# Optimization experiments

Measured on AMD Instinct MI355X. Metric: run time of the kernel, lower is better.

## Reference

```python
import jax, jax.numpy as jnp
import numpy as np


def setup_inputs() -> dict:
    key = jax.random.key(0)
    k1, k2, k3, k4, k5 = jax.random.split(key, 5)
    B, S, H, NL = 256, 128, 768, 2
    return {
        "t_logits": jax.random.normal(k1, (B, NL), dtype=jnp.float32),
        "s_logits": jax.random.normal(k2, (B, NL), dtype=jnp.float32),
        "t_features": jax.random.normal(k3, (B, S, H), dtype=jnp.float32),
        "s_features": jax.random.normal(k4, (B, S, H), dtype=jnp.float32),
        "labels": jax.random.randint(k5, (B,), 0, NL, dtype=jnp.int64),
        "k": 5,
        "temperature": 4,
    }


def reference(t_logits, s_logits, t_features, s_features, labels, k, temperature):
    B = s_features.shape[0]
    D = s_features.shape[1] * s_features.shape[2]  # flattened feature dim S*H
    T = jnp.asarray(temperature, dtype=s_logits.dtype)

    # train_loss: standard cross-entropy computed inside the student model
    logp = jax.nn.log_softmax(s_logits, axis=-1)
    train_loss = -jnp.mean(jnp.take_along_axis(logp, labels[:, None].astype(jnp.int32), axis=1))

    # soft_loss: KL(batchmean) between temperature-softened teacher/student
    soft_targets = jax.nn.softmax(t_logits / T, axis=-1)
    log_probs = jax.nn.log_softmax(s_logits / T, axis=-1)
    soft_loss = jnp.sum(soft_targets * (jnp.log(soft_targets) - log_probs)) / B * T * T

    # distill_loss: per-sample squared distances to label-matched teacher
    # features, take k nearest (self included, dist 0), sum of per-neighbor
    # MSE = sqdist / D.
    tf = t_features.reshape(B, -1)
    sf = s_features.reshape(B, -1)
    # ||s_i - t_j||^2 via GEMM: [B, B]
    sq = (jnp.sum(sf * sf, axis=1)[:, None]
          + jnp.sum(tf * tf, axis=1)[None, :]
          - 2.0 * sf @ tf.T)
    sq = jnp.maximum(sq, 0.0)
    same = labels[:, None] == labels[None, :]
    masked = jnp.where(same, sq, jnp.inf)
    neg_top, _ = jax.lax.top_k(-masked, k)  # k smallest distances per row
    vals = -neg_top
    valid = jnp.isfinite(vals)  # handles groups smaller than k
    distill_loss = jnp.sum(jnp.where(valid, vals, 0.0)) / D

    return train_loss, soft_loss, distill_loss
```

## Files before the change

kernel.cpp:

```cpp
#include <hip/hip_runtime.h>
#include <math.h>


#define BM 128
#define BN 128
#define BKF 32
#define NS 8

typedef __attribute__((ext_vector_type(8))) short short8;
typedef __attribute__((ext_vector_type(4))) float f32x4;

__device__ inline void async16(const float* g, float* l) {
    __builtin_amdgcn_global_load_lds(
        (const __attribute__((address_space(1))) void*)g,
        (__attribute__((address_space(3))) void*)l,
        16, 0, 0);
}

__device__ inline unsigned pack_trunc(float a, float b) {
    return (__float_as_uint(a) >> 16) | (__float_as_uint(b) & 0xffff0000u);
}

union U8 { short8 v; unsigned u[4]; };

__global__ __launch_bounds__(256) void gemm_dot_kernel(const float* __restrict__ S,
                                                       const float* __restrict__ T,
                                                       float* __restrict__ part,
                                                       float* __restrict__ spart,
                                                       float* __restrict__ tpart,
                                                       int B, int K, int KC) {
    __shared__ __align__(16) float As[BM * BKF];
    __shared__ __align__(16) float Bs[BN * BKF];

    const int tid  = threadIdx.x;
    const int i0   = blockIdx.x * BM;
    const int j0   = blockIdx.y * BN;
    const int bz   = blockIdx.z;
    const int kbeg = bz * KC;
    const int kend = kbeg + KC;

    const int lane = tid & 63;
    const int wid  = tid >> 6;
    const int wm   = wid >> 1;
    const int wn   = wid & 1;
    const int l15  = lane & 15;
    const int quad = lane >> 4;

    const int rl = lane >> 3;
    const int p  = lane & 7;
    const float* srcA[4];
    const float* srcB[4];
    float* dstA[4];
    float* dstB[4];
    #pragma unroll
    for (int j = 0; j < 4; ++j) {
        const int c   = wid * 4 + j;
        const int row = c * 8 + rl;
        const int g   = p ^ (row & 7);
        int gi = i0 + row; if (gi >= B) gi = B - 1;
        int gj = j0 + row; if (gj >= B) gj = B - 1;
        srcA[j] = S + (size_t)gi * K + kbeg + g * 4;
        srcB[j] = T + (size_t)gj * K + kbeg + g * 4;
        dstA[j] = &As[c * 256];
        dstB[j] = &Bs[c * 256];
    }

    int aoff[4], boff[4];
    #pragma unroll
    for (int t = 0; t < 4; ++t) {
        const int ra = wm * 64 + t * 16 + l15;
        aoff[t] = ra * BKF + (((2 * quad) ^ (ra & 7)) * 4);
        const int rb = wn * 64 + t * 16 + l15;
        boff[t] = rb * BKF + (((2 * quad) ^ (rb & 7)) * 4);
    }

    const bool doS = (blockIdx.y == 0);
    const bool doT = (blockIdx.x == 0);
    const int  rn  = tid >> 1;
    const int  hn  = tid & 1;

    f32x4 acc[4][4] = {};
    float pns = 0.f, pnt = 0.f;

    for (int kb = kbeg; kb < kend; kb += BKF) {
        __syncthreads();
        #pragma unroll
        for (int j = 0; j < 4; ++j) {
            async16(srcA[j], dstA[j]);
            async16(srcB[j], dstB[j]);
            srcA[j] += BKF;
            srcB[j] += BKF;
        }
        __syncthreads();

        if (doS) {
            #pragma unroll
            for (int j = 0; j < 4; ++j) {
                const int pos = hn * 4 + ((j + rn) & 3);
                f32x4 v = *(const f32x4*)&As[rn * BKF + pos * 4];
                pns += v.x * v.x + v.y * v.y + v.z * v.z + v.w * v.w;
            }
        }
        if (doT) {
            #pragma unroll
            for (int j = 0; j < 4; ++j) {
                const int pos = hn * 4 + ((j + rn) & 3);
                f32x4 v = *(const f32x4*)&Bs[rn * BKF + pos * 4];
                pnt += v.x * v.x + v.y * v.y + v.z * v.z + v.w * v.w;
            }
        }

        short8 af[4], bf[4];
        #pragma unroll
        for (int t = 0; t < 4; ++t) {
            f32x4 va = *(const f32x4*)&As[aoff[t]];
            f32x4 vb = *(const f32x4*)&As[aoff[t] ^ 4];
            U8 u;
            u.u[0] = pack_trunc(va.x, va.y);
            u.u[1] = pack_trunc(va.z, va.w);
            u.u[2] = pack_trunc(vb.x, vb.y);
            u.u[3] = pack_trunc(vb.z, vb.w);
            af[t] = u.v;
        }
        #pragma unroll
        for (int t = 0; t < 4; ++t) {
            f32x4 va = *(const f32x4*)&Bs[boff[t]];
            f32x4 vb = *(const f32x4*)&Bs[boff[t] ^ 4];
            U8 u;
            u.u[0] = pack_trunc(va.x, va.y);
            u.u[1] = pack_trunc(va.z, va.w);
            u.u[2] = pack_trunc(vb.x, vb.y);
            u.u[3] = pack_trunc(vb.z, vb.w);
            bf[t] = u.v;
        }
        #pragma unroll
        for (int mi = 0; mi < 4; ++mi)
            #pragma unroll
            for (int ni = 0; ni < 4; ++ni)
                acc[mi][ni] = __builtin_amdgcn_mfma_f32_16x16x32_bf16(
                    af[mi], bf[ni], acc[mi][ni], 0, 0, 0);
    }

    float* outp = part + (size_t)bz * B * B;
    #pragma unroll
    for (int mi = 0; mi < 4; ++mi) {
        #pragma unroll
        for (int ni = 0; ni < 4; ++ni) {
            #pragma unroll
            for (int r = 0; r < 4; ++r) {
                const int ig = i0 + wm * 64 + mi * 16 + quad * 4 + r;
                const int jg = j0 + wn * 64 + ni * 16 + l15;
                if (ig < B && jg < B)
                    outp[(size_t)ig * B + jg] = acc[mi][ni][r];
            }
        }
    }

    if (doS) {
        float v = pns + __shfl_xor(pns, 1, 64);
        if (hn == 0 && i0 + rn < B) spart[(size_t)bz * B + i0 + rn] = v;
    }
    if (doT) {
        float v = pnt + __shfl_xor(pnt, 1, 64);
        if (hn == 0 && j0 + rn < B) tpart[(size_t)bz * B + j0 + rn] = v;
    }
}

__global__ __launch_bounds__(256) void reduce_kernel(const float* __restrict__ part,
                                                     const float* __restrict__ spart,
                                                     const float* __restrict__ tpart,
                                                     float* __restrict__ part2,
                                                     float* __restrict__ snorm2,
                                                     float* __restrict__ tnorm2,
                                                     int n, int B, int gz) {
    const int s  = blockIdx.y;
    const int bx = blockIdx.x;
    const int t  = threadIdx.x;
    if ((int)bx * 256 < n) {
        const int idx = bx * 256 + t;
        if (idx < n) {
            float a = 0.f;
            for (int z = s; z < gz; z += NS)
                a += part[(size_t)z * n + idx];
            part2[(size_t)s * n + idx] = a;
        }
    } else {
        if (t < B) {
            float a = 0.f, b = 0.f;
            for (int z = s; z < gz; z += NS) {
                a += spart[(size_t)z * B + t];
                b += tpart[(size_t)z * B + t];
            }
            snorm2[s * B + t] = a;
            tnorm2[s * B + t] = b;
        }
    }
}

__global__ __launch_bounds__(256) void tail_kernel(const float* __restrict__ part2,
                                                   const float* __restrict__ snorm2,
                                                   const float* __restrict__ tnorm2,
                                                   const float* __restrict__ t_logits,
                                                   const float* __restrict__ s_logits,
                                                   const int* __restrict__ labels,
                                                   const int* __restrict__ kp,
                                                   const int* __restrict__ tp,
                                                   float* __restrict__ rowsum,
                                                   int* __restrict__ counter,
                                                   float* __restrict__ out,
                                                   int B, int K, int NL) {
    const int i   = blockIdx.x;
    const int tid = threadIdx.x;
    const size_t BB = (size_t)B * B;

    __shared__ float svals[256];
    __shared__ float rv[256];
    __shared__ int   ri[256];
    __shared__ int   lastf;

    float v = INFINITY;
    if (tid < B && labels[i] == labels[tid]) {
        float dt = 0.f, sn = 0.f, tn = 0.f;
        #pragma unroll
        for (int s = 0; s < NS; ++s) {
            dt += part2[(size_t)s * BB + (size_t)i * B + tid];
            sn += snorm2[s * B + i];
            tn += tnorm2[s * B + tid];
        }
        v = fmaxf(sn + tn - 2.0f * dt, 0.0f);
    }
    svals[tid] = v;
    __syncthreads();

    const int k = kp[0];
    float sum = 0.0f;
    for (int it = 0; it < k; ++it) {
        rv[tid] = svals[tid];
        ri[tid] = tid;
        __syncthreads();
        #pragma unroll
        for (int s = 128; s > 0; s >>= 1) {
            if (tid < s) {
                if (rv[tid + s] < rv[tid]) { rv[tid] = rv[tid + s]; ri[tid] = ri[tid + s]; }
            }
            __syncthreads();
        }
        if (tid == 0) {
            if (rv[0] < 3.0e38f) sum += rv[0];
            svals[ri[0]] = INFINITY;
        }
        __syncthreads();
    }

    if (tid == 0) {
        rowsum[i] = sum;
        __threadfence();
        lastf = (atomicAdd(counter, 1) == B - 1) ? 1 : 0;
    }
    __syncthreads();
    if (!lastf) return;

    __threadfence();
    const float Tv = (float)tp[0];
    float rs = (tid < B) ? rowsum[tid] : 0.f;
    float ce = 0.0f, kl = 0.0f;
    for (int s = tid; s < B; s += 256) {
        const float* sl = s_logits + (size_t)s * NL;
        const float* tl = t_logits + (size_t)s * NL;
        float mx = -INFINITY;
        for (int c = 0; c < NL; ++c) mx = fmaxf(mx, sl[c]);
        float se = 0.0f;
        for (int c = 0; c < NL; ++c) se += expf(sl[c] - mx);
        ce += logf(se) + mx - sl[labels[s]];

        float mxs = -INFINITY, mxt = -INFINITY;
        for (int c = 0; c < NL; ++c) {
            mxs = fmaxf(mxs, sl[c] / Tv);
            mxt = fmaxf(mxt, tl[c] / Tv);
        }
        float ses = 0.0f, set = 0.0f;
        for (int c = 0; c < NL; ++c) {
            ses += expf(sl[c] / Tv - mxs);
            set += expf(tl[c] / Tv - mxt);
        }
        float lses = logf(ses) + mxs;
        float lset = logf(set) + mxt;
        for (int c = 0; c < NL; ++c) {
            float lst = tl[c] / Tv - lset;
            float ls  = sl[c] / Tv - lses;
            kl += expf(lst) * (lst - ls);
        }
    }
    #pragma unroll
    for (int off = 32; off > 0; off >>= 1) {
        ce += __shfl_down(ce, off, 64);
        kl += __shfl_down(kl, off, 64);
        rs += __shfl_down(rs, off, 64);
    }
    __shared__ float wce[4], wkl[4], wrs[4];
    if ((tid & 63) == 0) { wce[tid >> 6] = ce; wkl[tid >> 6] = kl; wrs[tid >> 6] = rs; }
    __syncthreads();
    if (tid == 0) {
        out[0] = (wce[0] + wce[1] + wce[2] + wce[3]) / (float)B;
        out[1] = (wkl[0] + wkl[1] + wkl[2] + wkl[3]) / (float)B * Tv * Tv;
        out[2] = (wrs[0] + wrs[1] + wrs[2] + wrs[3]) / (float)K;
    }
}

extern "C" void kernel_launch(void* const* d_in, const int* in_sizes, int n_in,
                              void* d_out, int out_size, void* d_ws, size_t ws_size,
                              hipStream_t stream) {
    const float* t_logits = (const float*)d_in[0];
    const float* s_logits = (const float*)d_in[1];
    const float* t_feat   = (const float*)d_in[2];
    const float* s_feat   = (const float*)d_in[3];
    const int*   labels   = (const int*)d_in[4];
    const int*   kp       = (const int*)d_in[5];
    const int*   tp       = (const int*)d_in[6];
    float* out = (float*)d_out;

    const int B  = in_sizes[4];
    const int NL = in_sizes[0] / B;
    const int K  = in_sizes[2] / B;
    const size_t BB = (size_t)B * B;

    const size_t avail = ws_size / 4;
    const int cands[] = {192, 256, 128, 96, 64, 48, 32, 24, 16, 12, 8, 6, 4, 3, 2, 1};
    int gz = 1;
    for (int ci = 0; ci < 16; ++ci) {
        const int g = cands[ci];
        if (K % (g * BKF) != 0) continue;
        const size_t need = (size_t)g * BB + (size_t)NS * BB
                          + 2 * (size_t)g * B + 2 * (size_t)NS * B + B + 1;
        if (need <= avail) { gz = g; break; }
    }
    const int KC = K / gz;

    float* ws      = (float*)d_ws;
    float* part    = ws;
    float* part2   = part + (size_t)gz * BB;
    float* spart   = part2 + (size_t)NS * BB;
    float* tpart   = spart + (size_t)gz * B;
    float* snorm2  = tpart + (size_t)gz * B;
    float* tnorm2  = snorm2 + (size_t)NS * B;
    float* rowsum  = tnorm2 + (size_t)NS * B;
    int*   counter = (int*)(rowsum + B);

    hipMemsetAsync(counter, 0, sizeof(int), stream);

    dim3 grid((B + BM - 1) / BM, (B + BN - 1) / BN, gz);
    gemm_dot_kernel<<<grid, 256, 0, stream>>>(s_feat, t_feat, part, spart, tpart,
                                              B, K, KC);

    dim3 grid2((unsigned)(BB / 256 + 1), NS);
    reduce_kernel<<<grid2, 256, 0, stream>>>(part, spart, tpart, part2,
                                             snorm2, tnorm2, (int)BB, B, gz);

    tail_kernel<<<B, 256, 0, stream>>>(part2, snorm2, tnorm2, t_logits, s_logits,
                                       labels, kp, tp, rowsum, counter, out,
                                       B, K, NL);
}
```

Measured before the change: 277.1 us.

## Double-buffer GEMM LDS loads, drop reduce kernel, fold split-K sum into tail

The GEMM now double-buffers its LDS tiles: it prefetches the next K-slice with async global-to-LDS loads while the MFMAs run on the current one, which removes one barrier per iteration. The separate reduce kernel and the memset are removed. The counter is zeroed inside the GEMM, and the tail kernel sums all gz split-K partials directly. This saves two launches and a full intermediate write and read, but each tail thread now performs gz strided loads. It also assumes the counter reset is visible before the tail runs, which stream ordering provides.

```diff
diff --git a/kernel.cpp b/kernel.cpp
--- a/kernel.cpp
+++ b/kernel.cpp
@@ -5,7 +5,7 @@
 #define BM 128
 #define BN 128
 #define BKF 32
-#define NS 8
+#define STAGE (BM * BKF)
 
 typedef __attribute__((ext_vector_type(8))) short short8;
 typedef __attribute__((ext_vector_type(4))) float f32x4;
@@ -28,9 +28,9 @@
                                                        float* __restrict__ part,
                                                        float* __restrict__ spart,
                                                        float* __restrict__ tpart,
+                                                       int* __restrict__ counter,
                                                        int B, int K, int KC) {
-    __shared__ __align__(16) float As[BM * BKF];
-    __shared__ __align__(16) float Bs[BN * BKF];
+    extern __shared__ __align__(16) float smem[];
 
     const int tid  = threadIdx.x;
     const int i0   = blockIdx.x * BM;
@@ -39,6 +39,9 @@
     const int kbeg = bz * KC;
     const int kend = kbeg + KC;
 
+    if (blockIdx.x == 0 && blockIdx.y == 0 && bz == 0 && tid == 0)
+        *counter = 0;
+
     const int lane = tid & 63;
     const int wid  = tid >> 6;
     const int wm   = wid >> 1;
@@ -50,8 +53,7 @@
     const int p  = lane & 7;
     const float* srcA[4];
     const float* srcB[4];
-    float* dstA[4];
-    float* dstB[4];
+    int dstOff[4];
     #pragma unroll
     for (int j = 0; j < 4; ++j) {
         const int c   = wid * 4 + j;
@@ -61,8 +63,7 @@
         int gj = j0 + row; if (gj >= B) gj = B - 1;
         srcA[j] = S + (size_t)gi * K + kbeg + g * 4;
         srcB[j] = T + (size_t)gj * K + kbeg + g * 4;
-        dstA[j] = &As[c * 256];
-        dstB[j] = &Bs[c * 256];
+        dstOff[j] = c * 256;
     }
 
     int aoff[4], boff[4];
@@ -82,16 +83,36 @@
     f32x4 acc[4][4] = {};
     float pns = 0.f, pnt = 0.f;
 
+    {
+        float* As0 = smem;
+        float* Bs0 = smem + STAGE;
+        #pragma unroll
+        for (int j = 0; j < 4; ++j) {
+            async16(srcA[j], &As0[dstOff[j]]);
+            async16(srcB[j], &Bs0[dstOff[j]]);
+            srcA[j] += BKF;
+            srcB[j] += BKF;
+        }
+    }
+
+    int par = 0;
     for (int kb = kbeg; kb < kend; kb += BKF) {
         __syncthreads();
-        #pragma unroll
-        for (int j = 0; j < 4; ++j) {
-            async16(srcA[j], dstA[j]);
-            async16(srcB[j], dstB[j]);
-            srcA[j] += BKF;
-            srcB[j] += BKF;
-        }
-        __syncthreads();
+
+        if (kb + BKF < kend) {
+            float* Asn = smem + (par ^ 1) * 2 * STAGE;
+            float* Bsn = Asn + STAGE;
+            #pragma unroll
+            for (int j = 0; j < 4; ++j) {
+                async16(srcA[j], &Asn[dstOff[j]]);
+                async16(srcB[j], &Bsn[dstOff[j]]);
+                srcA[j] += BKF;
+                srcB[j] += BKF;
+            }
+        }
+
+        const float* As = smem + par * 2 * STAGE;
+        const float* Bs = As + STAGE;
 
         if (doS) {
             #pragma unroll
@@ -139,6 +160,8 @@
             for (int ni = 0; ni < 4; ++ni)
                 acc[mi][ni] = __builtin_amdgcn_mfma_f32_16x16x32_bf16(
                     af[mi], bf[ni], acc[mi][ni], 0, 0, 0);
+
+        par ^= 1;
     }
 
     float* outp = part + (size_t)bz * B * B;
@@ -166,40 +189,9 @@
     }
 }
 
-__global__ __launch_bounds__(256) void reduce_kernel(const float* __restrict__ part,
-                                                     const float* __restrict__ spart,
-                                                     const float* __restrict__ tpart,
-                                                     float* __restrict__ part2,
-                                                     float* __restrict__ snorm2,
-                                                     float* __restrict__ tnorm2,
-                                                     int n, int B, int gz) {
-    const int s  = blockIdx.y;
-    const int bx = blockIdx.x;
-    const int t  = threadIdx.x;
-    if ((int)bx * 256 < n) {
-        const int idx = bx * 256 + t;
-        if (idx < n) {
-            float a = 0.f;
-            for (int z = s; z < gz; z += NS)
-                a += part[(size_t)z * n + idx];
-            part2[(size_t)s * n + idx] = a;
-        }
-    } else {
-        if (t < B) {
-            float a = 0.f, b = 0.f;
-            for (int z = s; z < gz; z += NS) {
-                a += spart[(size_t)z * B + t];
-                b += tpart[(size_t)z * B + t];
-            }
-            snorm2[s * B + t] = a;
-            tnorm2[s * B + t] = b;
-        }
-    }
-}
-
-__global__ __launch_bounds__(256) void tail_kernel(const float* __restrict__ part2,
-                                                   const float* __restrict__ snorm2,
-                                                   const float* __restrict__ tnorm2,
+__global__ __launch_bounds__(256) void tail_kernel(const float* __restrict__ part,
+                                                   const float* __restrict__ spart,
+                                                   const float* __restrict__ tpart,
                                                    const float* __restrict__ t_logits,
                                                    const float* __restrict__ s_logits,
                                                    const int* __restrict__ labels,
@@ -208,7 +200,7 @@
                                                    float* __restrict__ rowsum,
                                                    int* __restrict__ counter,
                                                    float* __restrict__ out,
-                                                   int B, int K, int NL) {
+                                                   int B, int K, int NL, int gz) {
     const int i   = blockIdx.x;
     const int tid = threadIdx.x;
     const size_t BB = (size_t)B * B;
@@ -216,18 +208,48 @@
     __shared__ float svals[256];
     __shared__ float rv[256];
     __shared__ int   ri[256];
+    __shared__ float red[4];
+    __shared__ float snv;
     __shared__ int   lastf;
 
+    float sp = 0.f;
+    for (int z = tid; z < gz; z += 256) sp += spart[(size_t)z * B + i];
+    #pragma unroll
+    for (int off = 32; off > 0; off >>= 1) sp += __shfl_down(sp, off, 64);
+    if ((tid & 63) == 0) red[tid >> 6] = sp;
+    __syncthreads();
+    if (tid == 0) snv = red[0] + red[1] + red[2] + red[3];
+    __syncthreads();
+    const float sn = snv;
+
     float v = INFINITY;
-    if (tid < B && labels[i] == labels[tid]) {
-        float dt = 0.f, sn = 0.f, tn = 0.f;
-        #pragma unroll
-        for (int s = 0; s < NS; ++s) {
-            dt += part2[(size_t)s * BB + (size_t)i * B + tid];
-            sn += snorm2[s * B + i];
-            tn += tnorm2[s * B + tid];
-        }
-        v = fmaxf(sn + tn - 2.0f * dt, 0.0f);
+    if (tid < B) {
+        const float* pp = part + (size_t)i * B + tid;
+        const float* tq = tpart + tid;
+        float d0=0.f,d1=0.f,d2=0.f,d3=0.f,d4=0.f,d5=0.f,d6=0.f,d7=0.f;
+        float tn = 0.f;
+        int z = 0;
+        for (; z + 8 <= gz; z += 8) {
+            d0 += pp[(size_t)(z+0) * BB];
+            d1 += pp[(size_t)(z+1) * BB];
+            d2 += pp[(size_t)(z+2) * BB];
+            d3 += pp[(size_t)(z+3) * BB];
+            d4 += pp[(size_t)(z+4) * BB];
+            d5 += pp[(size_t)(z+5) * BB];
+            d6 += pp[(size_t)(z+6) * BB];
+            d7 += pp[(size_t)(z+7) * BB];
+            tn += tq[(size_t)(z+0) * B] + tq[(size_t)(z+1) * B]
+                + tq[(size_t)(z+2) * B] + tq[(size_t)(z+3) * B]
+                + tq[(size_t)(z+4) * B] + tq[(size_t)(z+5) * B]
+                + tq[(size_t)(z+6) * B] + tq[(size_t)(z+7) * B];
+        }
+        float dt = ((d0+d1)+(d2+d3)) + ((d4+d5)+(d6+d7));
+        for (; z < gz; ++z) {
+            dt += pp[(size_t)z * BB];
+            tn += tq[(size_t)z * B];
+        }
+        if (labels[i] == labels[tid])
+            v = fmaxf(sn + tn - 2.0f * dt, 0.0f);
     }
     svals[tid] = v;
     __syncthreads();
@@ -330,33 +352,25 @@
     for (int ci = 0; ci < 16; ++ci) {
         const int g = cands[ci];
         if (K % (g * BKF) != 0) continue;
-        const size_t need = (size_t)g * BB + (size_t)NS * BB
-                          + 2 * (size_t)g * B + 2 * (size_t)NS * B + B + 1;
+        const size_t need = (size_t)g * BB + 2 * (size_t)g * B + B + 1;
         if (need <= avail) { gz = g; break; }
     }
     const int KC = K / gz;
 
     float* ws      = (float*)d_ws;
     float* part    = ws;
-    float* part2   = part + (size_t)gz * BB;
-    float* spart   = part2 + (size_t)NS * BB;
+    float* spart   = part + (size_t)gz * BB;
     float* tpart   = spart + (size_t)gz * B;
-    float* snorm2  = tpart + (size_t)gz * B;
-    float* tnorm2  = snorm2 + (size_t)NS * B;
-    float* rowsum  = tnorm2 + (size_t)NS * B;
+    float* rowsum  = tpart + (size_t)gz * B;
     int*   counter = (int*)(rowsum + B);
 
-    hipMemsetAsync(counter, 0, sizeof(int), stream);
-
     dim3 grid((B + BM - 1) / BM, (B + BN - 1) / BN, gz);
-    gemm_dot_kernel<<<grid, 256, 0, stream>>>(s_feat, t_feat, part, spart, tpart,
-                                              B, K, KC);
-
-    dim3 grid2((unsigned)(BB / 256 + 1), NS);
-    reduce_kernel<<<grid2, 256, 0, stream>>>(part, spart, tpart, part2,
-                                             snorm2, tnorm2, (int)BB, B, gz);
-
-    tail_kernel<<<B, 256, 0, stream>>>(part2, snorm2, tnorm2, t_logits, s_logits,
+    const size_t lds_bytes = 4 * STAGE * sizeof(float);
+    gemm_dot_kernel<<<grid, 256, lds_bytes, stream>>>(s_feat, t_feat, part,
+                                                      spart, tpart, counter,
+                                                      B, K, KC);
+
+    tail_kernel<<<B, 256, 0, stream>>>(part, spart, tpart, t_logits, s_logits,
                                        labels, kp, tp, rowsum, counter, out,
-                                       B, K, NL);
-}
+                                       B, K, NL, gz);
+}
```

Measured after the change: 272.3 us. No clear change (-1.7%).
